# Performance work log

Hardware: AMD Instinct MI355X
Metric: run time of the kernel (lower is better)

## Reference

```python
import jax, jax.numpy as jnp
import numpy as np

N, D = 2048, 64
H, W = 128, 128
NEAR, RADIUS_CLIP, BLUR = 0.01, 3.0, 0.3
A_MIN, A_MAX = 1.0 / 255.0, 0.999


def setup_inputs():
    key = jax.random.key(0)
    k = jax.random.split(key, 6)
    xy = jax.random.uniform(k[0], (N, 2), minval=-1.2, maxval=1.2)
    zz = jax.random.uniform(k[1], (N, 1), minval=3.0, maxval=5.0)
    means = jnp.concatenate([xy, zz], axis=1).astype(jnp.float32)
    quats = jax.random.normal(k[2], (N, 4), dtype=jnp.float32)
    scales = jax.random.normal(k[3], (N, 3), dtype=jnp.float32) * 0.3 - 2.2  # log-scales
    opacities = jax.random.normal(k[4], (N,), dtype=jnp.float32) * 0.5 + 1.0  # logits
    gs_features = jax.random.normal(k[5], (N, D), dtype=jnp.float32) * 0.5
    c2o = jnp.eye(4, dtype=jnp.float32)
    K = jnp.array([[200.0, 0.0, 64.0], [0.0, 200.0, 64.0], [0.0, 0.0, 1.0]], dtype=jnp.float32)
    return dict(means=means, quats=quats, scales=scales, opacities=opacities,
                gs_features=gs_features, c2o=c2o, K=K, width=W, height=H)


def _quat_to_rot(q):
    q = q / jnp.linalg.norm(q, axis=-1, keepdims=True)
    w, x, y, z = q[:, 0], q[:, 1], q[:, 2], q[:, 3]
    r0 = jnp.stack([1 - 2 * (y * y + z * z), 2 * (x * y - w * z), 2 * (x * z + w * y)], -1)
    r1 = jnp.stack([2 * (x * y + w * z), 1 - 2 * (x * x + z * z), 2 * (y * z - w * x)], -1)
    r2 = jnp.stack([2 * (x * z - w * y), 2 * (y * z + w * x), 1 - 2 * (x * x + y * y)], -1)
    return jnp.stack([r0, r1, r2], -2)  # [N,3,3]


def _rasterize(means, quats, log_scales, opac_logits, colors, viewmat, K, width, height):
    Rv, tv = viewmat[:3, :3], viewmat[:3, 3]
    fx, fy, cx, cy = K[0, 0], K[1, 1], K[0, 2], K[1, 2]
    mc = means @ Rv.T + tv                      # camera-space means [N,3]
    x, y, z = mc[:, 0], mc[:, 1], mc[:, 2]
    # 3D covariance Sigma = R S S^T R^T, rotated into camera frame
    M = _quat_to_rot(quats) * jnp.exp(log_scales)[:, None, :]
    cov_w = M @ jnp.swapaxes(M, 1, 2)           # [N,3,3]
    cov_c = jnp.einsum('ij,njk,lk->nil', Rv, cov_w, Rv)
    # perspective (EWA) Jacobian [N,2,3]
    rz = 1.0 / z
    zero = jnp.zeros_like(z)
    J = jnp.stack([jnp.stack([fx * rz, zero, -fx * x * rz * rz], -1),
                   jnp.stack([zero, fy * rz, -fy * y * rz * rz], -1)], -2)
    cov2d = jnp.einsum('nij,njk,nlk->nil', J, cov_c, J)
    a = cov2d[:, 0, 0] + BLUR
    b = cov2d[:, 0, 1]
    c = cov2d[:, 1, 1] + BLUR
    det = a * c - b * b
    cA, cB, cC = c / det, -b / det, a / det     # conic = inverse 2D covariance
    mx = fx * x * rz + cx
    my = fy * y * rz + cy
    # cull: behind near plane, degenerate, or projected 3-sigma radius below radius_clip
    lam_max = 0.5 * (a + c) + jnp.sqrt(jnp.maximum(0.25 * (a - c) ** 2 + b * b, 1e-12))
    radius = 3.0 * jnp.sqrt(lam_max)
    valid = (z > NEAR) & (det > 0) & (radius > RADIUS_CLIP)
    opac = jax.nn.sigmoid(opac_logits)
    # global front-to-back depth order (single camera)
    order = jnp.argsort(z)
    mx, my, cA, cB, cC = mx[order], my[order], cA[order], cB[order], cC[order]
    opac, valid, colors = opac[order], valid[order], colors[order]
    # per pixel-gaussian evaluation, [H,W,N]
    px = jnp.arange(width, dtype=means.dtype) + 0.5
    py = jnp.arange(height, dtype=means.dtype) + 0.5
    dx = px[None, :, None] - mx[None, None, :]
    dy = py[:, None, None] - my[None, None, :]
    sigma = 0.5 * (cA * dx * dx + cC * dy * dy) + cB * dx * dy
    alpha = jnp.minimum(opac * jnp.exp(-sigma), A_MAX)
    alpha = jnp.where((sigma >= 0) & valid & (alpha >= A_MIN), alpha, 0.0)
    # front-to-back alpha compositing: exclusive transmittance cumprod
    Tcum = jnp.cumprod(1.0 - alpha, axis=-1)
    T_excl = jnp.concatenate([jnp.ones_like(Tcum[..., :1]), Tcum[..., :-1]], axis=-1)
    out = jnp.einsum('hwn,nd->hwd', alpha * T_excl, colors)
    return out[None]  # [1,H,W,D]


def reference(means, quats, scales, opacities, gs_features, c2o, K, width, height):
    viewmat = jnp.linalg.inv(c2o)
    return _rasterize(means, quats, scales, opacities, gs_features, viewmat, K, width, height)
```

## Files before the change

### kernel.cpp

```cpp
#include <hip/hip_runtime.h>

constexpr int NG  = 2048;
constexpr int DF  = 64;
constexpr int IW  = 128;
constexpr int IH  = 128;
constexpr int NZ  = 8;
constexpr int RB  = 1024;
constexpr int CAP = 1024;

#define P_NEAR 0.01f
#define P_BLUR 0.3f
#define P_AMIN (1.0f/255.0f)
#define P_AMAX 0.999f

constexpr int L_T    = 0;
constexpr int L_CNT  = 512;
constexpr int L_SIDX = 528;
constexpr int L_OVL  = L_SIDX + CAP;
constexpr int L_PRM  = L_OVL;
constexpr int L_KEYS = L_PRM + CAP * 8;
constexpr int L_ACC  = L_OVL;
constexpr int ACC_ST = 66;
constexpr int L_TOTAL = L_OVL + NZ * 64 * ACC_ST;

__device__ inline void invert4x4(const float* m, float* inv) {
    inv[0]  =  m[5]*m[10]*m[15] - m[5]*m[11]*m[14] - m[9]*m[6]*m[15] + m[9]*m[7]*m[14] + m[13]*m[6]*m[11] - m[13]*m[7]*m[10];
    inv[4]  = -m[4]*m[10]*m[15] + m[4]*m[11]*m[14] + m[8]*m[6]*m[15] - m[8]*m[7]*m[14] - m[12]*m[6]*m[11] + m[12]*m[7]*m[10];
    inv[8]  =  m[4]*m[9]*m[15]  - m[4]*m[11]*m[13] - m[8]*m[5]*m[15] + m[8]*m[7]*m[13] + m[12]*m[5]*m[11] - m[12]*m[7]*m[9];
    inv[12] = -m[4]*m[9]*m[14]  + m[4]*m[10]*m[13] + m[8]*m[5]*m[14] - m[8]*m[6]*m[13] - m[12]*m[5]*m[10] + m[12]*m[6]*m[9];
    inv[1]  = -m[1]*m[10]*m[15] + m[1]*m[11]*m[14] + m[9]*m[2]*m[15] - m[9]*m[3]*m[14] - m[13]*m[2]*m[11] + m[13]*m[3]*m[10];
    inv[5]  =  m[0]*m[10]*m[15] - m[0]*m[11]*m[14] - m[8]*m[2]*m[15] + m[8]*m[3]*m[14] + m[12]*m[2]*m[11] - m[12]*m[3]*m[10];
    inv[9]  = -m[0]*m[9]*m[15]  + m[0]*m[11]*m[13] + m[8]*m[1]*m[15] - m[8]*m[3]*m[13] - m[12]*m[1]*m[11] + m[12]*m[3]*m[9];
    inv[13] =  m[0]*m[9]*m[14]  - m[0]*m[10]*m[13] - m[8]*m[1]*m[14] + m[8]*m[2]*m[13] + m[12]*m[1]*m[10] - m[12]*m[2]*m[9];
    inv[2]  =  m[1]*m[6]*m[15]  - m[1]*m[7]*m[14]  - m[5]*m[2]*m[15] + m[5]*m[3]*m[14] + m[13]*m[2]*m[7]  - m[13]*m[3]*m[6];
    inv[6]  = -m[0]*m[6]*m[15]  + m[0]*m[7]*m[14]  + m[4]*m[2]*m[15] - m[4]*m[3]*m[14] - m[12]*m[2]*m[7]  + m[12]*m[3]*m[6];
    inv[10] =  m[0]*m[5]*m[15]  - m[0]*m[7]*m[13]  - m[4]*m[1]*m[15] + m[4]*m[3]*m[13] + m[12]*m[1]*m[7]  - m[12]*m[3]*m[5];
    inv[14] = -m[0]*m[5]*m[14]  + m[0]*m[6]*m[13]  + m[4]*m[1]*m[14] - m[4]*m[2]*m[13] - m[12]*m[1]*m[6]  + m[12]*m[2]*m[5];
    inv[3]  = -m[1]*m[6]*m[11]  + m[1]*m[7]*m[10]  + m[5]*m[2]*m[11] - m[5]*m[3]*m[10] - m[9]*m[2]*m[7]   + m[9]*m[3]*m[6];
    inv[7]  =  m[0]*m[6]*m[11]  - m[0]*m[7]*m[10]  - m[4]*m[2]*m[11] + m[4]*m[3]*m[10] + m[8]*m[2]*m[7]   - m[8]*m[3]*m[6];
    inv[11] = -m[0]*m[5]*m[11]  + m[0]*m[7]*m[9]   + m[4]*m[1]*m[11] - m[4]*m[3]*m[9]  - m[8]*m[1]*m[7]   + m[8]*m[3]*m[5];
    inv[15] =  m[0]*m[5]*m[10]  - m[0]*m[6]*m[9]   - m[4]*m[1]*m[10] + m[4]*m[2]*m[9]  + m[8]*m[1]*m[6]   - m[8]*m[2]*m[5];
    float det = m[0]*inv[0] + m[1]*inv[4] + m[2]*inv[8] + m[3]*inv[12];
    det = 1.0f / det;
    #pragma unroll
    for (int i = 0; i < 16; ++i) inv[i] *= det;
}

__global__ __launch_bounds__(RB, 4) void fused_render_kernel(
    const float* __restrict__ means,  const float* __restrict__ quats,
    const float* __restrict__ scales, const float* __restrict__ opac_logits,
    const float* __restrict__ colors, const float* __restrict__ c2o,
    const float* __restrict__ Kmat,   float* __restrict__ out)
{
    extern __shared__ float lds[];
    int*                cnt  = (int*)(lds + L_CNT);
    int*                sidx = (int*)(lds + L_SIDX);
    unsigned long long* keys = (unsigned long long*)(lds + L_KEYS);
    float4*             prm4 = (float4*)(lds + L_PRM);

    const int tid  = threadIdx.x;
    const int lane = tid & 63;
    const int wv16 = tid >> 6;
    const int sz   = wv16 >> 1;
    const int hh   = wv16 & 1;
    const int tile = blockIdx.x;
    const int tx = (tile & 15) * 8;
    const int ty = (tile >> 4) * 8;
    const float px = tx + (lane & 7) + 0.5f;
    const float py = ty + (lane >> 3) + 0.5f;
    const float cxt = tx + 4.0f, cyt = ty + 4.0f;

    if (tid == 0) *cnt = 0;
    __syncthreads();

    {
        float inv[16];
        {
            float m[16];
            #pragma unroll
            for (int t = 0; t < 16; ++t) m[t] = c2o[t];
            invert4x4(m, inv);
        }
        const float fx = Kmat[0], fy = Kmat[4], cx = Kmat[2], cy = Kmat[5];

        #pragma unroll
        for (int c = 0; c < NG / RB; ++c) {
            const int g = c * RB + tid;
            float mx = means[g*3+0], my = means[g*3+1], mz = means[g*3+2];
            float X = inv[0]*mx + inv[1]*my + inv[2]*mz  + inv[3];
            float Y = inv[4]*mx + inv[5]*my + inv[6]*mz  + inv[7];
            float Z = inv[8]*mx + inv[9]*my + inv[10]*mz + inv[11];

            float qw = quats[g*4+0], qx = quats[g*4+1], qy = quats[g*4+2], qz = quats[g*4+3];
            float qn = rsqrtf(qw*qw + qx*qx + qy*qy + qz*qz);
            qw *= qn; qx *= qn; qy *= qn; qz *= qn;
            float R00 = 1.f - 2.f*(qy*qy + qz*qz), R01 = 2.f*(qx*qy - qw*qz), R02 = 2.f*(qx*qz + qw*qy);
            float R10 = 2.f*(qx*qy + qw*qz), R11 = 1.f - 2.f*(qx*qx + qz*qz), R12 = 2.f*(qy*qz - qw*qx);
            float R20 = 2.f*(qx*qz - qw*qy), R21 = 2.f*(qy*qz + qw*qx), R22 = 1.f - 2.f*(qx*qx + qy*qy);

            float s0 = expf(scales[g*3+0]), s1 = expf(scales[g*3+1]), s2 = expf(scales[g*3+2]);
            float M00 = R00*s0, M01 = R01*s1, M02 = R02*s2;
            float M10 = R10*s0, M11 = R11*s1, M12 = R12*s2;
            float M20 = R20*s0, M21 = R21*s1, M22 = R22*s2;

            float V00 = M00*M00 + M01*M01 + M02*M02;
            float V01 = M00*M10 + M01*M11 + M02*M12;
            float V02 = M00*M20 + M01*M21 + M02*M22;
            float V11 = M10*M10 + M11*M11 + M12*M12;
            float V12 = M10*M20 + M11*M21 + M12*M22;
            float V22 = M20*M20 + M21*M21 + M22*M22;

            float Rv[3][3] = {{inv[0],inv[1],inv[2]},{inv[4],inv[5],inv[6]},{inv[8],inv[9],inv[10]}};
            float Vm[3][3] = {{V00,V01,V02},{V01,V11,V12},{V02,V12,V22}};
            float Tm[3][3], C[3][3];
            #pragma unroll
            for (int r = 0; r < 3; ++r)
                #pragma unroll
                for (int cc = 0; cc < 3; ++cc)
                    Tm[r][cc] = Rv[r][0]*Vm[0][cc] + Rv[r][1]*Vm[1][cc] + Rv[r][2]*Vm[2][cc];
            #pragma unroll
            for (int r = 0; r < 3; ++r)
                #pragma unroll
                for (int cc = 0; cc < 3; ++cc)
                    C[r][cc] = Tm[r][0]*Rv[cc][0] + Tm[r][1]*Rv[cc][1] + Tm[r][2]*Rv[cc][2];

            float rz = 1.0f / Z;
            float j00 = fx*rz, j02 = -fx*X*rz*rz;
            float j11 = fy*rz, j12 = -fy*Y*rz*rz;

            float c00 = j00*j00*C[0][0] + 2.f*j00*j02*C[0][2] + j02*j02*C[2][2];
            float c01 = j00*j11*C[0][1] + j00*j12*C[0][2] + j02*j11*C[1][2] + j02*j12*C[2][2];
            float c11 = j11*j11*C[1][1] + 2.f*j11*j12*C[1][2] + j12*j12*C[2][2];

            float a = c00 + P_BLUR;
            float b = c01;
            float cc_ = c11 + P_BLUR;
            float det = a*cc_ - b*b;

            float pmx = fx*X*rz + cx;
            float pmy = fy*Y*rz + cy;

            float lam = 0.5f*(a + cc_) + sqrtf(fmaxf(0.25f*(a - cc_)*(a - cc_) + b*b, 1e-12f));
            float radius = 3.0f * sqrtf(lam);
            bool valid = (Z > P_NEAR) && (det > 0.0f) && (radius > 3.0f);

            float op = 1.0f / (1.0f + expf(-opac_logits[g]));

            bool sel = false;
            float cA = 0.f, cB = 0.f, cC2 = 0.f;
            if (valid) {
                float rdet = 1.0f / det;
                cA = cc_ * rdet; cB = -b * rdet; cC2 = a * rdet;
                float smax = logf(255.0f * op);
                if (smax > 0.f) {
                    float rx = sqrtf(2.f * a   * smax) * 1.0001f + 1e-3f;
                    float ry = sqrtf(2.f * cc_ * smax) * 1.0001f + 1e-3f;
                    sel = (fabsf(pmx - cxt) <= rx + 3.5f) && (fabsf(pmy - cyt) <= ry + 3.5f);
                }
            }

            unsigned long long m = __ballot(sel);
            int wbase = 0;
            if (lane == 0 && m) wbase = atomicAdd(cnt, (int)__popcll(m));
            wbase = __shfl(wbase, 0);
            if (sel) {
                int pos = wbase + (int)__popcll(m & ((1ull << lane) - 1ull));
                if (pos < CAP) {
                    prm4[pos*2]   = make_float4(pmx, pmy, cA, cB);
                    prm4[pos*2+1] = make_float4(cC2, op, __int_as_float(g), 0.f);
                    keys[pos] = ((unsigned long long)__float_as_uint(Z) << 32) | (unsigned)g;
                }
            }
        }
    }
    __syncthreads();
    int L = *cnt;
    if (L > CAP) L = CAP;

    {
        int padL = (L + 1) & ~1;
        if (tid < padL - L) keys[L + tid] = ~0ull;
        __syncthreads();
        const ulonglong2* k2 = (const ulonglong2*)keys;
        if (tid < L) {
            unsigned long long kk = keys[tid];
            int rank = 0;
            #pragma unroll 2
            for (int c = 0; c < padL / 2; ++c) {
                ulonglong2 q = k2[c];
                rank += (q.x < kk) + (q.y < kk);
            }
            sidx[rank] = tid;
        }
    }
    __syncthreads();

    float acc[32];
    #pragma unroll
    for (int f = 0; f < 32; ++f) acc[f] = 0.f;
    float T = 1.0f;

    {
        const int r0 = (sz * L) >> 3;
        const int r1 = ((sz + 1) * L) >> 3;
        const float4* cph = (const float4*)colors + hh * 8;
        if (r1 > r0) {
            int k = sidx[r0];
            float4 e0 = prm4[k*2], e1 = prm4[k*2+1];
            for (int r = r0; r < r1; ++r) {
                int kn = (r + 1 < r1) ? sidx[r + 1] : k;
                float4 n0 = prm4[kn*2], n1 = prm4[kn*2+1];

                float dx = px - e0.x, dy = py - e0.y;
                float sig = 0.5f*(e0.z*dx*dx + e1.x*dy*dy) + e0.w*dx*dy;
                float al = fminf(e1.y * __expf(-sig), P_AMAX);
                al = (sig >= 0.f && al >= P_AMIN) ? al : 0.f;

                if (__ballot(al > 0.f)) {
                    float wv = T * al;
                    const float4* crow = cph + (size_t)(unsigned)__float_as_int(e1.z) * 16;
                    #pragma unroll
                    for (int q = 0; q < 8; ++q) {
                        float4 cv = crow[q];
                        acc[4*q+0] = fmaf(wv, cv.x, acc[4*q+0]);
                        acc[4*q+1] = fmaf(wv, cv.y, acc[4*q+1]);
                        acc[4*q+2] = fmaf(wv, cv.z, acc[4*q+2]);
                        acc[4*q+3] = fmaf(wv, cv.w, acc[4*q+3]);
                    }
                    T *= (1.f - al);
                    if (!__ballot(T >= 1e-6f)) break;
                }
                e0 = n0; e1 = n1; k = kn;
            }
        }
    }

    if (hh == 0) lds[L_T + sz*64 + lane] = T;
    __syncthreads();
    {
        float* ab = lds + L_ACC + (size_t)(sz * 64 + lane) * ACC_ST + hh * 32;
        #pragma unroll
        for (int q = 0; q < 16; ++q)
            *(float2*)(ab + 2*q) = make_float2(acc[2*q], acc[2*q+1]);
    }
    __syncthreads();

    {
        int p  = tid >> 4;
        int f0 = (tid & 15) * 4;
        float r0, r1, r2, r3;
        const float* ab = lds + L_ACC + (size_t)((NZ-1)*64 + p) * ACC_ST + f0;
        { float2 u = *(const float2*)ab, v = *(const float2*)(ab + 2);
          r0 = u.x; r1 = u.y; r2 = v.x; r3 = v.y; }
        #pragma unroll
        for (int s = NZ - 2; s >= 0; --s) {
            float Ts = lds[L_T + s*64 + p];
            const float* as_ = lds + L_ACC + (size_t)(s*64 + p) * ACC_ST + f0;
            float2 u = *(const float2*)as_, v = *(const float2*)(as_ + 2);
            r0 = fmaf(Ts, r0, u.x); r1 = fmaf(Ts, r1, u.y);
            r2 = fmaf(Ts, r2, v.x); r3 = fmaf(Ts, r3, v.y);
        }
        int pyg = ty + (p >> 3), pxg = tx + (p & 7);
        float* op_ = out + (size_t)(pyg * IW + pxg) * DF + f0;
        *(float4*)op_ = make_float4(r0, r1, r2, r3);
    }
}

extern "C" void kernel_launch(void* const* d_in, const int* in_sizes, int n_in,
                              void* d_out, int out_size, void* d_ws, size_t ws_size,
                              hipStream_t stream) {
    const float* means  = (const float*)d_in[0];
    const float* quats  = (const float*)d_in[1];
    const float* scales = (const float*)d_in[2];
    const float* opac   = (const float*)d_in[3];
    const float* colors = (const float*)d_in[4];
    const float* c2o    = (const float*)d_in[5];
    const float* Kmat   = (const float*)d_in[6];
    float* out = (float*)d_out;
    (void)d_ws; (void)ws_size;

    (void)hipFuncSetAttribute((const void*)fused_render_kernel,
                              hipFuncAttributeMaxDynamicSharedMemorySize,
                              L_TOTAL * 4);

    fused_render_kernel<<<IH*IW/64, RB, L_TOTAL*4, stream>>>(
        means, quats, scales, opac, colors, c2o, Kmat, out);
}
```

Measured before the change: 115.2 us.

## Split fused renderer into preprocess, global sort, segmented raster and combine kernels

Replaces the single fused kernel with four kernels when workspace is large enough. Projection runs once per gaussian instead of being repeated per tile, and a global rank sort scatters the sorted parameters. Rasterization splits each tile's depth list across two blocks of 16 slices each, and a final combine kernel merges the back segment using the front segment's transmittance. This aims to raise parallelism and drop redundant per-tile preprocessing, at the cost of extra launches, global-memory round trips and larger per-thread accumulator register pressure. The old fused path is kept as a fallback.

Result: slower. 242.9 us (+110.9%).

```diff
diff --git a/kernel.cpp b/kernel.cpp
--- a/kernel.cpp
+++ b/kernel.cpp
@@ -4,24 +4,11 @@
 constexpr int DF  = 64;
 constexpr int IW  = 128;
 constexpr int IH  = 128;
-constexpr int NZ  = 8;
-constexpr int RB  = 1024;
-constexpr int CAP = 1024;
 
 #define P_NEAR 0.01f
 #define P_BLUR 0.3f
 #define P_AMIN (1.0f/255.0f)
 #define P_AMAX 0.999f
-
-constexpr int L_T    = 0;
-constexpr int L_CNT  = 512;
-constexpr int L_SIDX = 528;
-constexpr int L_OVL  = L_SIDX + CAP;
-constexpr int L_PRM  = L_OVL;
-constexpr int L_KEYS = L_PRM + CAP * 8;
-constexpr int L_ACC  = L_OVL;
-constexpr int ACC_ST = 66;
-constexpr int L_TOTAL = L_OVL + NZ * 64 * ACC_ST;
 
 __device__ inline void invert4x4(const float* m, float* inv) {
     inv[0]  =  m[5]*m[10]*m[15] - m[5]*m[11]*m[14] - m[9]*m[6]*m[15] + m[9]*m[7]*m[14] + m[13]*m[6]*m[11] - m[13]*m[7]*m[10];
@@ -46,6 +33,20 @@
     for (int i = 0; i < 16; ++i) inv[i] *= det;
 }
 
+constexpr int NZ  = 8;
+constexpr int RB  = 1024;
+constexpr int CAP = 1024;
+
+constexpr int L_T    = 0;
+constexpr int L_CNT  = 512;
+constexpr int L_SIDX = 528;
+constexpr int L_OVL  = L_SIDX + CAP;
+constexpr int L_PRM  = L_OVL;
+constexpr int L_KEYS = L_PRM + CAP * 8;
+constexpr int L_ACC  = L_OVL;
+constexpr int ACC_ST = 66;
+constexpr int L_TOTAL = L_OVL + NZ * 64 * ACC_ST;
+
 __global__ __launch_bounds__(RB, 4) void fused_render_kernel(
     const float* __restrict__ means,  const float* __restrict__ quats,
     const float* __restrict__ scales, const float* __restrict__ opac_logits,
@@ -266,6 +267,282 @@
     }
 }
 
+constexpr int NSL    = 16;
+constexpr int NSEG   = 2;
+constexpr int AST    = 12;
+constexpr int NTILES = 256;
+
+constexpr size_t WS_TMPA = 0;
+constexpr size_t WS_TMPB = WS_TMPA + NG*4;
+constexpr size_t WS_ZB   = WS_TMPB + NG*4;
+constexpr size_t WS_SA   = WS_ZB   + NG;
+constexpr size_t WS_SB   = WS_SA   + NG*4;
+constexpr size_t WS_SG   = WS_SB   + NG*4;
+constexpr size_t WS_T0   = WS_SG   + NG;
+constexpr size_t WS_ACC1 = WS_T0   + NTILES*64;
+constexpr size_t WS_TOTAL= WS_ACC1 + (size_t)NTILES*64*DF;
+
+__global__ __launch_bounds__(64) void preprocess_kernel(
+    const float* __restrict__ means,  const float* __restrict__ quats,
+    const float* __restrict__ scales, const float* __restrict__ opac_logits,
+    const float* __restrict__ c2o,    const float* __restrict__ Kmat,
+    float* __restrict__ ws)
+{
+    const int g = blockIdx.x * 64 + threadIdx.x;
+
+    float inv[16];
+    {
+        float m[16];
+        #pragma unroll
+        for (int t = 0; t < 16; ++t) m[t] = c2o[t];
+        invert4x4(m, inv);
+    }
+    const float fx = Kmat[0], fy = Kmat[4], cx = Kmat[2], cy = Kmat[5];
+
+    float mx = means[g*3+0], my = means[g*3+1], mz = means[g*3+2];
+    float X = inv[0]*mx + inv[1]*my + inv[2]*mz  + inv[3];
+    float Y = inv[4]*mx + inv[5]*my + inv[6]*mz  + inv[7];
+    float Z = inv[8]*mx + inv[9]*my + inv[10]*mz + inv[11];
+
+    float qw = quats[g*4+0], qx = quats[g*4+1], qy = quats[g*4+2], qz = quats[g*4+3];
+    float qn = rsqrtf(qw*qw + qx*qx + qy*qy + qz*qz);
+    qw *= qn; qx *= qn; qy *= qn; qz *= qn;
+    float R00 = 1.f - 2.f*(qy*qy + qz*qz), R01 = 2.f*(qx*qy - qw*qz), R02 = 2.f*(qx*qz + qw*qy);
+    float R10 = 2.f*(qx*qy + qw*qz), R11 = 1.f - 2.f*(qx*qx + qz*qz), R12 = 2.f*(qy*qz - qw*qx);
+    float R20 = 2.f*(qx*qz - qw*qy), R21 = 2.f*(qy*qz + qw*qx), R22 = 1.f - 2.f*(qx*qx + qy*qy);
+
+    float s0 = expf(scales[g*3+0]), s1 = expf(scales[g*3+1]), s2 = expf(scales[g*3+2]);
+    float M00 = R00*s0, M01 = R01*s1, M02 = R02*s2;
+    float M10 = R10*s0, M11 = R11*s1, M12 = R12*s2;
+    float M20 = R20*s0, M21 = R21*s1, M22 = R22*s2;
+
+    float V00 = M00*M00 + M01*M01 + M02*M02;
+    float V01 = M00*M10 + M01*M11 + M02*M12;
+    float V02 = M00*M20 + M01*M21 + M02*M22;
+    float V11 = M10*M10 + M11*M11 + M12*M12;
+    float V12 = M10*M20 + M11*M21 + M12*M22;
+    float V22 = M20*M20 + M21*M21 + M22*M22;
+
+    float Rv[3][3] = {{inv[0],inv[1],inv[2]},{inv[4],inv[5],inv[6]},{inv[8],inv[9],inv[10]}};
+    float Vm[3][3] = {{V00,V01,V02},{V01,V11,V12},{V02,V12,V22}};
+    float Tm[3][3], C[3][3];
+    #pragma unroll
+    for (int r = 0; r < 3; ++r)
+        #pragma unroll
+        for (int cc = 0; cc < 3; ++cc)
+            Tm[r][cc] = Rv[r][0]*Vm[0][cc] + Rv[r][1]*Vm[1][cc] + Rv[r][2]*Vm[2][cc];
+    #pragma unroll
+    for (int r = 0; r < 3; ++r)
+        #pragma unroll
+        for (int cc = 0; cc < 3; ++cc)
+            C[r][cc] = Tm[r][0]*Rv[cc][0] + Tm[r][1]*Rv[cc][1] + Tm[r][2]*Rv[cc][2];
+
+    float rz = 1.0f / Z;
+    float j00 = fx*rz, j02 = -fx*X*rz*rz;
+    float j11 = fy*rz, j12 = -fy*Y*rz*rz;
+
+    float c00 = j00*j00*C[0][0] + 2.f*j00*j02*C[0][2] + j02*j02*C[2][2];
+    float c01 = j00*j11*C[0][1] + j00*j12*C[0][2] + j02*j11*C[1][2] + j02*j12*C[2][2];
+    float c11 = j11*j11*C[1][1] + 2.f*j11*j12*C[1][2] + j12*j12*C[2][2];
+
+    float a = c00 + P_BLUR;
+    float b = c01;
+    float cc_ = c11 + P_BLUR;
+    float det = a*cc_ - b*b;
+
+    float pmx = fx*X*rz + cx;
+    float pmy = fy*Y*rz + cy;
+
+    float lam = 0.5f*(a + cc_) + sqrtf(fmaxf(0.25f*(a - cc_)*(a - cc_) + b*b, 1e-12f));
+    float radius = 3.0f * sqrtf(lam);
+    bool valid = (Z > P_NEAR) && (det > 0.0f) && (radius > 3.0f);
+
+    float op = 1.0f / (1.0f + expf(-opac_logits[g]));
+
+    float cA = 0.f, cB = 0.f, cC2 = 0.f, rx = -1e9f, ry = -1e9f;
+    if (valid) {
+        float rdet = 1.0f / det;
+        cA = cc_ * rdet; cB = -b * rdet; cC2 = a * rdet;
+        float smax = logf(255.0f * op);
+        if (smax > 0.f) {
+            rx = sqrtf(2.f * a   * smax) * 1.0001f + 1e-3f;
+            ry = sqrtf(2.f * cc_ * smax) * 1.0001f + 1e-3f;
+        }
+    }
+
+    ((float4*)(ws + WS_TMPA))[g] = make_float4(pmx, pmy, cA, cB);
+    ((float4*)(ws + WS_TMPB))[g] = make_float4(cC2, op, rx, ry);
+    ((unsigned*)(ws + WS_ZB))[g] = __float_as_uint(Z);
+}
+
+__global__ __launch_bounds__(512) void sort_scatter_kernel(float* __restrict__ ws)
+{
+    __shared__ int cnt[8][64];
+    const int lane = threadIdx.x & 63;
+    const int part = threadIdx.x >> 6;
+    const int g = blockIdx.x * 64 + lane;
+    const unsigned* zb = (const unsigned*)(ws + WS_ZB);
+    const unsigned zk = zb[g];
+    const uint4* z4 = (const uint4*)zb;
+
+    int c = 0;
+    for (int i = part*64; i < part*64 + 64; ++i) {
+        uint4 q = z4[i];
+        const int j = i * 4;
+        c += (q.x < zk || (q.x == zk && j+0 < g)) ? 1 : 0;
+        c += (q.y < zk || (q.y == zk && j+1 < g)) ? 1 : 0;
+        c += (q.z < zk || (q.z == zk && j+2 < g)) ? 1 : 0;
+        c += (q.w < zk || (q.w == zk && j+3 < g)) ? 1 : 0;
+    }
+    cnt[part][lane] = c;
+    __syncthreads();
+    if (part == 0) {
+        int rank = 0;
+        #pragma unroll
+        for (int e = 0; e < 8; ++e) rank += cnt[e][lane];
+        ((float4*)(ws + WS_SA))[rank] = ((const float4*)(ws + WS_TMPA))[g];
+        ((float4*)(ws + WS_SB))[rank] = ((const float4*)(ws + WS_TMPB))[g];
+        ((int*)  (ws + WS_SG))[rank] = g;
+    }
+}
+
+__global__ __launch_bounds__(1024) void raster_kernel(
+    const float* __restrict__ colors, float* __restrict__ ws,
+    float* __restrict__ out)
+{
+    __shared__ float ureg[NSL*64*AST];
+    __shared__ float Tlds[NSL*64];
+    __shared__ int   s_wcnt[16];
+
+    const int tid  = threadIdx.x;
+    const int lane = tid & 63;
+    const int w    = tid >> 6;
+    const int b    = blockIdx.x;
+    const int tile = b & (NTILES - 1);
+    const int seg  = b >> 8;
+    const int tx = (tile & 15) * 8, ty = (tile >> 4) * 8;
+    const float px = tx + (lane & 7) + 0.5f;
+    const float py = ty + (lane >> 3) + 0.5f;
+    const float cxt = tx + 4.0f, cyt = ty + 4.0f;
+
+    float4* prm4 = (float4*)ureg;
+    const float4* sA = (const float4*)(ws + WS_SA);
+    const float4* sB = (const float4*)(ws + WS_SB);
+    const int*    sG = (const int*)  (ws + WS_SG);
+
+    int Lrun = 0;
+    #pragma unroll
+    for (int ch = 0; ch < NG/1024; ++ch) {
+        const int j = ch*1024 + tid;
+        float4 A = sA[j], B = sB[j];
+        bool sel = (fabsf(A.x - cxt) <= B.z + 3.5f) && (fabsf(A.y - cyt) <= B.w + 3.5f);
+        unsigned long long m = __ballot(sel);
+        if (lane == 0) s_wcnt[w] = (int)__popcll(m);
+        __syncthreads();
+        int pre = 0, tot = 0;
+        #pragma unroll
+        for (int e = 0; e < 16; ++e) { int cw = s_wcnt[e]; pre += (e < w) ? cw : 0; tot += cw; }
+        if (sel) {
+            int pos = Lrun + pre + (int)__popcll(m & ((1ull << lane) - 1ull));
+            if (pos < CAP) {
+                prm4[pos*2]   = A;
+                prm4[pos*2+1] = make_float4(B.x, B.y, __int_as_float(sG[j]), 0.f);
+            }
+        }
+        Lrun += tot;
+        __syncthreads();
+    }
+    const int L = (Lrun < CAP) ? Lrun : CAP;
+
+    float acc[64];
+    #pragma unroll
+    for (int i = 0; i < 64; ++i) acc[i] = 0.f;
+    float T = 1.0f;
+    {
+        const int v  = seg * NSL + w;
+        const int r0 = (v * L) >> 5;
+        const int r1 = ((v + 1) * L) >> 5;
+        const float4* colors4 = (const float4*)colors;
+        if (r1 > r0) {
+            float4 e0 = prm4[2*r0], e1 = prm4[2*r0+1];
+            for (int r = r0; r < r1; ++r) {
+                const int rn = (r + 1 < r1) ? r + 1 : r;
+                float4 n0 = prm4[2*rn], n1 = prm4[2*rn+1];
+
+                float dx = px - e0.x, dy = py - e0.y;
+                float sig = 0.5f*(e0.z*dx*dx + e1.x*dy*dy) + e0.w*dx*dy;
+                float al = fminf(e1.y * __expf(-sig), P_AMAX);
+                al = (sig >= 0.f && al >= P_AMIN) ? al : 0.f;
+
+                if (__ballot(al > 0.f)) {
+                    float wv = T * al;
+                    const float4* crow = colors4 + (size_t)(unsigned)__float_as_int(e1.z) * (DF/4);
+                    #pragma unroll
+                    for (int q = 0; q < 16; ++q) {
+                        float4 cv = crow[q];
+                        acc[4*q+0] = fmaf(wv, cv.x, acc[4*q+0]);
+                        acc[4*q+1] = fmaf(wv, cv.y, acc[4*q+1]);
+                        acc[4*q+2] = fmaf(wv, cv.z, acc[4*q+2]);
+                        acc[4*q+3] = fmaf(wv, cv.w, acc[4*q+3]);
+                    }
+                    T *= (1.f - al);
+                    if (!__ballot(T >= 1e-6f)) break;
+                }
+                e0 = n0; e1 = n1;
+            }
+        }
+    }
+
+    Tlds[w*64 + lane] = T;
+    __syncthreads();
+
+    if (seg == 0 && tid < 64) {
+        float tp = 1.f;
+        #pragma unroll
+        for (int s = 0; s < NSL; ++s) tp *= Tlds[s*64 + tid];
+        ws[WS_T0 + tile*64 + tid] = tp;
+    }
+
+    #pragma unroll
+    for (int pass = 0; pass < 8; ++pass) {
+        float* ab = ureg + (w*64 + lane) * AST;
+        *(float4*)(ab)     = make_float4(acc[pass*8+0], acc[pass*8+1], acc[pass*8+2], acc[pass*8+3]);
+        *(float4*)(ab + 4) = make_float4(acc[pass*8+4], acc[pass*8+5], acc[pass*8+6], acc[pass*8+7]);
+        __syncthreads();
+        if (tid < 512) {
+            const int p = tid >> 3, f = tid & 7;
+            float r = ureg[((NSL-1)*64 + p)*AST + f];
+            #pragma unroll
+            for (int s = NSL-2; s >= 0; --s)
+                r = fmaf(Tlds[s*64 + p], r, ureg[(s*64 + p)*AST + f]);
+            const int pxg = tx + (p & 7), pyg = ty + (p >> 3);
+            const int fi = pass*8 + f;
+            if (seg == 0) out[(size_t)(pyg*IW + pxg)*DF + fi] = r;
+            else          ws[WS_ACC1 + ((size_t)tile*64 + p)*DF + fi] = r;
+        }
+        __syncthreads();
+    }
+}
+
+__global__ __launch_bounds__(1024) void combine_kernel(
+    float* __restrict__ out, const float* __restrict__ ws)
+{
+    const int tile = blockIdx.x;
+    const int p  = threadIdx.x >> 4;
+    const int f0 = (threadIdx.x & 15) * 4;
+    const int pxg = (tile & 15)*8 + (p & 7);
+    const int pyg = (tile >> 4)*8 + (p >> 3);
+    const float T0 = ws[WS_T0 + tile*64 + p];
+    const float4 a1 = *(const float4*)(ws + WS_ACC1 + ((size_t)tile*64 + p)*DF + f0);
+    float4* o = (float4*)(out + (size_t)(pyg*IW + pxg)*DF + f0);
+    float4 v = *o;
+    v.x = fmaf(T0, a1.x, v.x);
+    v.y = fmaf(T0, a1.y, v.y);
+    v.z = fmaf(T0, a1.z, v.z);
+    v.w = fmaf(T0, a1.w, v.w);
+    *o = v;
+}
+
 extern "C" void kernel_launch(void* const* d_in, const int* in_sizes, int n_in,
                               void* d_out, int out_size, void* d_ws, size_t ws_size,
                               hipStream_t stream) {
@@ -277,12 +554,18 @@
     const float* c2o    = (const float*)d_in[5];
     const float* Kmat   = (const float*)d_in[6];
     float* out = (float*)d_out;
-    (void)d_ws; (void)ws_size;
-
-    (void)hipFuncSetAttribute((const void*)fused_render_kernel,
-                              hipFuncAttributeMaxDynamicSharedMemorySize,
-                              L_TOTAL * 4);
-
-    fused_render_kernel<<<IH*IW/64, RB, L_TOTAL*4, stream>>>(
-        means, quats, scales, opac, colors, c2o, Kmat, out);
-}
+
+    if (ws_size >= WS_TOTAL * sizeof(float)) {
+        float* ws = (float*)d_ws;
+        preprocess_kernel  <<<NG/64,        64,   0, stream>>>(means, quats, scales, opac, c2o, Kmat, ws);
+        sort_scatter_kernel<<<NG/64,        512,  0, stream>>>(ws);
+        raster_kernel      <<<NTILES*NSEG,  1024, 0, stream>>>(colors, ws, out);
+        combine_kernel     <<<NTILES,       1024, 0, stream>>>(out, ws);
+    } else {
+        (void)hipFuncSetAttribute((const void*)fused_render_kernel,
+                                  hipFuncAttributeMaxDynamicSharedMemorySize,
+                                  L_TOTAL * 4);
+        fused_render_kernel<<<IH*IW/64, RB, L_TOTAL*4, stream>>>(
+            means, quats, scales, opac, colors, c2o, Kmat, out);
+    }
+}
```
